# Kernel optimization log

Hardware: AMD Instinct MI355X
Metric: run time of the kernel (lower is better)

## Reference

```python
import jax, jax.numpy as jnp
import numpy as np

N_HEADS = 16
HEAD_DIM = 64
D_MODEL = N_HEADS * HEAD_DIM
NEG_INF = -10000.0


def setup_inputs() -> dict:
    key = jax.random.key(0)
    ks = jax.random.split(key, 6)
    B, S = 2, 2048
    std = 0.02
    return {
        "from_tensor": jax.random.normal(ks[0], (B, S, D_MODEL), dtype=jnp.float32),
        "to_tensor": jax.random.normal(ks[1], (B, S, D_MODEL), dtype=jnp.float32),
        "attention_mask": jnp.ones((B, S, S), dtype=jnp.int32),
        "Wq": jax.random.normal(ks[2], (D_MODEL, D_MODEL), dtype=jnp.float32) * std,
        "bq": jnp.zeros((D_MODEL,), dtype=jnp.float32),
        "Wk": jax.random.normal(ks[3], (D_MODEL, D_MODEL), dtype=jnp.float32) * std,
        "bk": jnp.zeros((D_MODEL,), dtype=jnp.float32),
        "Wv": jax.random.normal(ks[4], (D_MODEL, D_MODEL), dtype=jnp.float32) * std,
        "bv": jnp.zeros((D_MODEL,), dtype=jnp.float32),
    }


def reference(from_tensor, to_tensor, attention_mask, Wq, bq, Wk, bk, Wv, bv):
    B, F, _ = from_tensor.shape
    T = to_tensor.shape[1]
    # Dense QKV projections (no activation by default)
    q = from_tensor @ Wq + bq          # [B, F, N*H]
    k = to_tensor @ Wk + bk            # [B, T, N*H]
    v = to_tensor @ Wv + bv            # [B, T, N*H]
    # split heads -> [B, N, S, H]
    q = q.reshape(B, F, N_HEADS, HEAD_DIM).transpose(0, 2, 1, 3)
    k = k.reshape(B, T, N_HEADS, HEAD_DIM).transpose(0, 2, 1, 3)
    v = v.reshape(B, T, N_HEADS, HEAD_DIM).transpose(0, 2, 1, 3)
    # scaled dot-product scores [B, N, F, T]
    scores = jnp.einsum("bnfh,bnth->bnft", q, k) / jnp.sqrt(jnp.float32(HEAD_DIM))
    # additive mask: (1 - mask) * -10000, broadcast over heads
    adder = (1.0 - attention_mask.astype(jnp.float32))[:, None, :, :] * NEG_INF
    scores = scores + adder
    probs = jax.nn.softmax(scores, axis=-1)  # dropout is identity at inference
    ctx = jnp.einsum("bnft,bnth->bnfh", probs, v)  # [B, N, F, H]
    return ctx.transpose(0, 2, 1, 3).reshape(B, F, N_HEADS * HEAD_DIM)
```

## Files before the change

### kernel.cpp

```cpp
#include <hip/hip_runtime.h>
#include <hip/hip_bf16.h>

typedef unsigned short u16;
typedef __bf16 bf16x8 __attribute__((ext_vector_type(8)));
typedef float f32x4 __attribute__((ext_vector_type(4)));

#define D_MODEL 1024
#define NH 16
#define HD 64
#define SEQ 2048
#define BATCH 2

__device__ __forceinline__ f32x4 mfma16(bf16x8 a, bf16x8 b, f32x4 c) {
    return __builtin_amdgcn_mfma_f32_16x16x32_bf16(a, b, c, 0, 0, 0);
}

__device__ __forceinline__ u16 f2bf(float f) {
    __hip_bfloat16 h = __float2bfloat16(f);
    return *reinterpret_cast<u16*>(&h);
}

__device__ __forceinline__ unsigned cvt_pk_bf16(float lo, float hi) {
    unsigned r;
    asm("v_cvt_pk_bf16_f32 %0, %1, %2" : "=v"(r) : "v"(lo), "v"(hi));
    return r;
}

__device__ __forceinline__ void gload_lds16(const void* g, void* l) {
    __builtin_amdgcn_global_load_lds((__attribute__((address_space(1))) void*)g,
                                     (__attribute__((address_space(3))) void*)l,
                                     16, 0, 0);
}

__global__ __launch_bounds__(256) void prep_k(
    const float* __restrict__ X0, const float* __restrict__ X1,
    u16* __restrict__ Xqc, u16* __restrict__ Xkvc,
    const float* __restrict__ W0, const float* __restrict__ W1,
    const float* __restrict__ W2, u16* __restrict__ Wt,
    const int* __restrict__ mask, int* __restrict__ flags) {
    __shared__ __align__(16) u16 t[64][72];
    const int tid = threadIdx.x;
    int bid = blockIdx.x;

    if (bid < 4096) {
        int i = bid * 256 + tid;
        const float* src = X0; u16* dst = Xqc;
        if (i >= 524288) { src = X1; dst = Xkvc; i -= 524288; }
        const float4 a = ((const float4*)src)[i * 2];
        const float4 b = ((const float4*)src)[i * 2 + 1];
        union { u16 h[8]; uint4 v; } u;
        u.h[0] = f2bf(a.x); u.h[1] = f2bf(a.y); u.h[2] = f2bf(a.z); u.h[3] = f2bf(a.w);
        u.h[4] = f2bf(b.x); u.h[5] = f2bf(b.y); u.h[6] = f2bf(b.z); u.h[7] = f2bf(b.w);
        *(uint4*)(dst + i * 8) = u.v;
        return;
    }
    bid -= 4096;
    if (bid < 768) {
        const int z = bid >> 8, rem = bid & 255;
        const int bx = rem & 15, by = rem >> 4;
        const float* src = (z == 0) ? W0 : (z == 1 ? W1 : W2);
        u16* dst = Wt + (size_t)z * D_MODEL * D_MODEL;
        const int r0 = by * 64, c0 = bx * 64;
#pragma unroll
        for (int j = 0; j < 2; ++j) {
            int idx = j * 256 + tid;
            int rr = idx >> 3, cc = idx & 7;
            size_t base = (size_t)(r0 + rr) * D_MODEL + c0 + cc * 8;
            float4 a = *(const float4*)(src + base);
            float4 b = *(const float4*)(src + base + 4);
            union { u16 h[8]; uint4 v; } u;
            u.h[0] = f2bf(a.x); u.h[1] = f2bf(a.y); u.h[2] = f2bf(a.z); u.h[3] = f2bf(a.w);
            u.h[4] = f2bf(b.x); u.h[5] = f2bf(b.y); u.h[6] = f2bf(b.z); u.h[7] = f2bf(b.w);
            *(uint4*)&t[rr][cc * 8] = u.v;
        }
        __syncthreads();
#pragma unroll
        for (int j = 0; j < 2; ++j) {
            int idx = j * 256 + tid;
            int cc = idx >> 3, rr8 = idx & 7;
            union { u16 h[8]; uint4 v; } u;
#pragma unroll
            for (int e = 0; e < 8; ++e) u.h[e] = t[rr8 * 8 + e][cc];
            *(uint4*)(dst + (size_t)(c0 + cc) * D_MODEL + r0 + rr8 * 8) = u.v;
        }
        return;
    }
    bid -= 768;
    {
        const int ti = bid & 31, fi = (bid >> 5) & 15, b = bid >> 9;
        const int f = fi * 128 + (tid >> 1);
        const int4* p = (const int4*)(mask + ((size_t)(b * SEQ + f)) * SEQ + ti * 64 + (tid & 1) * 32);
        int ok = 1;
#pragma unroll
        for (int j = 0; j < 8; ++j) {
            int4 v = p[j];
            ok &= (v.x == 1) & (v.y == 1) & (v.z == 1) & (v.w == 1);
        }
        __shared__ int sflag;
        if (tid == 0) sflag = 1;
        __syncthreads();
        if (!ok) sflag = 0;
        __syncthreads();
        if (tid == 0) flags[(b * 16 + fi) * 32 + ti] = sflag;
    }
}

__global__ __launch_bounds__(256, 3) void qkv_gemm_k(
    const u16* __restrict__ Xq, const u16* __restrict__ Xkv,
    const u16* __restrict__ Wt,
    const float* __restrict__ bq, const float* __restrict__ bk,
    const float* __restrict__ bv,
    u16* __restrict__ Qb, u16* __restrict__ Kb, u16* __restrict__ Vt) {
    {
    }
    const int lbid = (int)blockIdx.x + 32 * (int)blockIdx.y + 256 * (int)blockIdx.z;
    const int xcd = lbid & 7, j = lbid >> 3;
    const int g = xcd * 3 + (j >> 5);
    const int bx = j & 31, by = g & 7, bz = g >> 3;

    const int z = bz;
    const u16* X = (z == 0) ? Xq : Xkv;
    const u16* Wz = Wt + (size_t)z * D_MODEL * D_MODEL;
    const float* bias = (z == 0) ? bq : (z == 1 ? bk : bv);
    const float scale = (z == 0) ? 0.1803368801111244f : 1.0f;

    __shared__ __align__(16) u16 As[128 * 32];
    __shared__ __align__(16) u16 Bs[128 * 32];

    const int tid = threadIdx.x;
    const int w = tid >> 6, lane = tid & 63;
    const int q = lane >> 4, c = lane & 15;
    const int m0 = bx * 128, n0 = by * 128;
    const int mw = (w & 1) * 64, nw = (w >> 1) * 64;

    f32x4 acc[4][4];
    const f32x4 z4 = {0.f, 0.f, 0.f, 0.f};
#pragma unroll
    for (int mi = 0; mi < 4; ++mi)
#pragma unroll
        for (int ni = 0; ni < 4; ++ni) acc[mi][ni] = z4;

    for (int kb = 0; kb < 32; ++kb) {
        const int k0 = kb * 32;
#pragma unroll
        for (int jj = 0; jj < 2; ++jj) {
            int i = jj * 256 + tid;
            int r = i >> 2, cc = i & 3;
            gload_lds16(X + (size_t)(m0 + r) * D_MODEL + k0 + cc * 8, As + i * 8);
            gload_lds16(Wz + (size_t)(n0 + r) * D_MODEL + k0 + cc * 8, Bs + i * 8);
        }
        __syncthreads();
        bf16x8 af[4], bfr[4];
#pragma unroll
        for (int mi = 0; mi < 4; ++mi)
            af[mi] = *(const bf16x8*)(As + (mw + mi * 16 + c) * 32 + q * 8);
#pragma unroll
        for (int ni = 0; ni < 4; ++ni)
            bfr[ni] = *(const bf16x8*)(Bs + (nw + ni * 16 + c) * 32 + q * 8);
#pragma unroll
        for (int mi = 0; mi < 4; ++mi)
#pragma unroll
            for (int ni = 0; ni < 4; ++ni)
                acc[mi][ni] = mfma16(af[mi], bfr[ni], acc[mi][ni]);
        __syncthreads();
    }

    if (z == 2) {
#pragma unroll
        for (int ni = 0; ni < 4; ++ni) {
            const int colg = n0 + nw + ni * 16 + c;
            const float bvv = bias[colg];
            const int head = colg >> 6, h = colg & 63;
#pragma unroll
            for (int mi = 0; mi < 4; ++mi) {
                const int rowg = m0 + mw + mi * 16 + q * 4;
                const int b = rowg >> 11, s = rowg & 2047;
                union { u16 h4[4]; uint2 v2; } pk;
#pragma unroll
                for (int r = 0; r < 4; ++r) pk.h4[r] = f2bf(acc[mi][ni][r] + bvv);
                *(uint2*)(Vt + (((size_t)(b * NH + head)) * HD + h) * SEQ + s) = pk.v2;
            }
        }
    } else {
        u16* outb = (z == 0) ? Qb : Kb;
#pragma unroll
        for (int ni = 0; ni < 4; ++ni) {
            const int colg = n0 + nw + ni * 16 + c;
            const float bvv = bias[colg];
            const int head = colg >> 6, h = colg & 63;
#pragma unroll
            for (int mi = 0; mi < 4; ++mi) {
                const int rowg = m0 + mw + mi * 16 + q * 4;
#pragma unroll
                for (int r = 0; r < 4; ++r) {
                    const int mrow = rowg + r;
                    const int b = mrow >> 11, s = mrow & 2047;
                    const float val = (acc[mi][ni][r] + bvv) * scale;
                    outb[(((size_t)(b * NH + head)) * SEQ + s) * HD + h] = f2bf(val);
                }
            }
        }
    }
}

#define SWZ(row, off) ((off) ^ (((row) & 7) << 3))
#define SK_OFF (128 * 128)
#define SV_OFF (SK_OFF + 64 * 128)
#define SMEM_BYTES (SV_OFF + 64 * 128)

__global__ __launch_bounds__(256, 4) void attn_k(
    const u16* __restrict__ Qb, const u16* __restrict__ Kb, const u16* __restrict__ Vt,
    const int* __restrict__ flags, const int* __restrict__ mask,
    float* __restrict__ O0, float* __restrict__ l0, float* __restrict__ l1,
    float* __restrict__ out) {
    __shared__ __align__(16) unsigned char smem[SMEM_BYTES];
    const int tid = threadIdx.x;
    const int w = tid >> 6, lane = tid & 63;
    const int q = lane >> 4, c = lane & 15;
    const int lbid = (int)blockIdx.x + 16 * ((int)blockIdx.y + 32 * (int)blockIdx.z);
    const int xcd = lbid & 7, jj = lbid >> 3;
    const int group = xcd * 8 + (jj >> 4);
    const int fi = jj & 15, bn = group & 31, ts = group >> 5;
    const int b = bn >> 4, n = bn & 15;
    const int f0 = fi * 128;

    u16* sQ = (u16*)(smem);
    u16* sK = (u16*)(smem + SK_OFF);
    u16* sV = (u16*)(smem + SV_OFF);
    u16* sP = sQ + w * 32 * 64;

#pragma unroll
    for (int j = 0; j < 4; ++j) {
        int i = j * 256 + tid;
        int r = i >> 3, cc = i & 7;
        uint4 v = *(const uint4*)(Qb + ((size_t)(bn * SEQ + f0 + r)) * HD + cc * 8);
        *(uint4*)(sQ + r * 64 + SWZ(r, cc * 8)) = v;
    }
    __syncthreads();

    bf16x8 qf[2][2];
#pragma unroll
    for (int ft = 0; ft < 2; ++ft)
#pragma unroll
        for (int kb = 0; kb < 2; ++kb)
            qf[ft][kb] = *(const bf16x8*)(sQ + (w * 32 + ft * 16 + c) * 64 + SWZ(c, kb * 32 + q * 8));
    __asm__ __volatile__("" ::: "memory");
    __builtin_amdgcn_s_waitcnt(0xC07F);
    __asm__ __volatile__("" ::: "memory");

    union { u16 h[8]; bf16x8 v; } one_u;
#pragma unroll
    for (int j = 0; j < 8; ++j) one_u.h[j] = 0x3F80;
    const bf16x8 ones = one_u.v;

    f32x4 O[2][4], accL[2];
    const f32x4 z4 = {0.f, 0.f, 0.f, 0.f};
    const f32x4 m10 = {-10.f, -10.f, -10.f, -10.f};
#pragma unroll
    for (int mi = 0; mi < 2; ++mi) {
        accL[mi] = z4;
#pragma unroll
        for (int hi = 0; hi < 4; ++hi) O[mi][hi] = z4;
    }
    const int* flagp = flags + (b * 16 + fi) * 32;

    const int it0 = ts * 16;
    for (int it = it0; it < it0 + 16; ++it) {
        const int t0 = it * 64;
#pragma unroll
        for (int j = 0; j < 2; ++j) {
            int i = j * 256 + tid;
            int r = i >> 3, cc = i & 7;
            uint4 kv = *(const uint4*)(Kb + ((size_t)(bn * SEQ + t0 + r)) * HD + cc * 8);
            uint4 vv = *(const uint4*)(Vt + ((size_t)(bn * HD + r)) * SEQ + t0 + cc * 8);
            const int so = r * 64 + SWZ(r, cc * 8);
            *(uint4*)(sK + so) = kv;
            *(uint4*)(sV + so) = vv;
        }
        __syncthreads();

        const int maskslow = (flagp[it] == 0);

#pragma unroll
        for (int mt = 0; mt < 4; ++mt) {
            bf16x8 kf0 = *(const bf16x8*)(sK + (mt * 16 + c) * 64 + SWZ(c, 0 + q * 8));
            bf16x8 kf1 = *(const bf16x8*)(sK + (mt * 16 + c) * 64 + SWZ(c, 32 + q * 8));
            f32x4 st[2];
            __builtin_amdgcn_s_setprio(1);
#pragma unroll
            for (int ft = 0; ft < 2; ++ft) {
                st[ft] = mfma16(kf0, qf[ft][0], m10);
                st[ft] = mfma16(kf1, qf[ft][1], st[ft]);
            }
            __builtin_amdgcn_s_setprio(0);
            if (maskslow) {
#pragma unroll
                for (int ft = 0; ft < 2; ++ft)
#pragma unroll
                    for (int r = 0; r < 4; ++r) {
                        const int fg = f0 + w * 32 + ft * 16 + c;
                        const int tg = t0 + mt * 16 + q * 4 + r;
                        const int mv = mask[((size_t)(b * SEQ + fg)) * SEQ + tg];
                        st[ft][r] += (1.0f - (float)mv) * (-10000.0f) * 1.4426950408889634f;
                    }
            }
#pragma unroll
            for (int ft = 0; ft < 2; ++ft) {
                uint2 v2;
                v2.x = cvt_pk_bf16(exp2f(st[ft][0]), exp2f(st[ft][1]));
                v2.y = cvt_pk_bf16(exp2f(st[ft][2]), exp2f(st[ft][3]));
                *(uint2*)(sP + (ft * 16 + c) * 64 + SWZ(c, mt * 16 + q * 4)) = v2;
            }
        }
        __asm__ __volatile__("" ::: "memory");
        __builtin_amdgcn_s_waitcnt(0xC07F);
        __asm__ __volatile__("" ::: "memory");

        __builtin_amdgcn_s_setprio(1);
#pragma unroll
        for (int kb = 0; kb < 2; ++kb) {
            bf16x8 pf0 = *(const bf16x8*)(sP + (0 * 16 + c) * 64 + SWZ(c, kb * 32 + q * 8));
            bf16x8 pf1 = *(const bf16x8*)(sP + (1 * 16 + c) * 64 + SWZ(c, kb * 32 + q * 8));
#pragma unroll
            for (int hi = 0; hi < 4; ++hi) {
                bf16x8 vf = *(const bf16x8*)(sV + (hi * 16 + c) * 64 + SWZ(c, kb * 32 + q * 8));
                O[0][hi] = mfma16(pf0, vf, O[0][hi]);
                O[1][hi] = mfma16(pf1, vf, O[1][hi]);
            }
            accL[0] = mfma16(pf0, ones, accL[0]);
            accL[1] = mfma16(pf1, ones, accL[1]);
        }
        __builtin_amdgcn_s_setprio(0);
        __syncthreads();
    }

    float* Odst = ts ? out : O0;
    float* ldst = ts ? l1 : l0;
#pragma unroll
    for (int mi = 0; mi < 2; ++mi)
#pragma unroll
        for (int hi = 0; hi < 4; ++hi)
#pragma unroll
            for (int r = 0; r < 4; ++r) {
                const int fg = f0 + w * 32 + mi * 16 + q * 4 + r;
                const int col = n * 64 + hi * 16 + c;
                Odst[((size_t)(b * SEQ + fg)) * D_MODEL + col] = O[mi][hi][r];
            }
    if (c == 0) {
#pragma unroll
        for (int mi = 0; mi < 2; ++mi)
#pragma unroll
            for (int r = 0; r < 4; ++r) {
                const int fg = f0 + w * 32 + mi * 16 + q * 4 + r;
                ldst[(size_t)bn * SEQ + fg] = accL[mi][r];
            }
    }
}

__global__ __launch_bounds__(256) void combine_k(const float* __restrict__ O0,
                                                 const float* __restrict__ l0,
                                                 const float* __restrict__ l1,
                                                 float* __restrict__ out) {
    const int i = blockIdx.x * 256 + threadIdx.x;
    const int bf = i >> 8;
    const int col = (i & 255) << 2;
    const int n = col >> 6;
    const int lidx = ((bf >> 11) * NH + n) * SEQ + (bf & (SEQ - 1));
    const float inv = 1.0f / (l0[lidx] + l1[lidx]);
    const float4 a = ((const float4*)O0)[i];
    const float4 cpart = ((const float4*)out)[i];
    float4 r;
    r.x = (a.x + cpart.x) * inv;
    r.y = (a.y + cpart.y) * inv;
    r.z = (a.z + cpart.z) * inv;
    r.w = (a.w + cpart.w) * inv;
    ((float4*)out)[i] = r;
}

__global__ __launch_bounds__(256) void signal_k(float* __restrict__ out, int n,
                                                float val) {
    const int i = blockIdx.x * 256 + threadIdx.x;
    if (i < n) out[i] = val;
}

extern "C" void kernel_launch(void* const* d_in, const int* in_sizes, int n_in,
                              void* d_out, int out_size, void* d_ws, size_t ws_size,
                              hipStream_t stream) {
    const float* Xs[2] = {nullptr, nullptr};
    const float* Wp[3] = {nullptr, nullptr, nullptr};
    const float* Bp[3] = {nullptr, nullptr, nullptr};
    const int* mask = nullptr;
    int nx = 0, nw = 0, nb = 0;
    for (int i = 0; i < n_in; ++i) {
        const long long sz = in_sizes[i];
        if (sz == (long long)BATCH * SEQ * D_MODEL) {
            if (nx < 2) Xs[nx++] = (const float*)d_in[i];
        } else if (sz == (long long)BATCH * SEQ * SEQ) {
            mask = (const int*)d_in[i];
        } else if (sz == (long long)D_MODEL * D_MODEL) {
            if (nw < 3) Wp[nw++] = (const float*)d_in[i];
        } else if (sz == (long long)D_MODEL) {
            if (nb < 3) Bp[nb++] = (const float*)d_in[i];
        }
    }
    float* outp = (float*)d_out;
    const size_t MB = 1024 * 1024;
    const size_t NEED = 47 * MB;

    if (ws_size < NEED || nx != 2 || nw != 3 || nb != 3 || !mask) {
        float code = 1000.0f + (float)(ws_size / MB)
                   + (nx != 2 ? 10000.0f : 0.f)
                   + (nw != 3 ? 20000.0f : 0.f)
                   + (nb != 3 ? 40000.0f : 0.f)
                   + (!mask   ? 80000.0f : 0.f);
        signal_k<<<(out_size + 255) / 256, 256, 0, stream>>>(outp, out_size, code);
        return;
    }

    char* ws = (char*)d_ws;
    u16* Xqc   = (u16*)(ws);
    u16* Xkvc  = (u16*)(ws + 8 * MB);
    u16* Wt    = (u16*)(ws + 16 * MB);
    u16* Qb    = (u16*)(ws + 22 * MB);
    u16* Kb    = (u16*)(ws + 30 * MB);
    u16* Vt    = (u16*)(ws + 38 * MB);
    int* flags = (int*)(ws + 46 * MB);
    float* O0 = (float*)(ws);
    float* l0 = (float*)(ws + 46 * MB + 16 * 1024);
    float* l1 = (float*)(ws + 46 * MB + 16 * 1024 + 256 * 1024);

    prep_k<<<5888, 256, 0, stream>>>(Xs[0], Xs[1], Xqc, Xkvc,
                                     Wp[0], Wp[1], Wp[2], Wt, mask, flags);
    qkv_gemm_k<<<dim3(32, 8, 3), 256, 0, stream>>>(Xqc, Xkvc, Wt,
                                                   Bp[0], Bp[1], Bp[2], Qb, Kb, Vt);
    attn_k<<<dim3(16, 32, 2), 256, 0, stream>>>(Qb, Kb, Vt, flags, mask,
                                                O0, l0, l1, outp);
    combine_k<<<4096, 256, 0, stream>>>(O0, l0, l1, outp);
}
```

Baseline: 222.1 us.

## Load K/V fragments directly from global into registers, drop LDS staging and barriers

The attention kernel no longer stages K and V tiles through shared memory. Each lane loads its MFMA operand fragments straight from global memory into registers, which removes the per-iteration __syncthreads barriers and cuts the LDS footprint to the Q/P area. The cost is that each of the four waves now fetches the same K/V data redundantly (relying on L1/L2), and register pressure rises. Because no other wave reads a given wave's P region, only a local waitcnt is kept at the loop end.

```diff
diff --git a/kernel.cpp b/kernel.cpp
--- a/kernel.cpp
+++ b/kernel.cpp
@@ -111,8 +111,6 @@
     const float* __restrict__ bq, const float* __restrict__ bk,
     const float* __restrict__ bv,
     u16* __restrict__ Qb, u16* __restrict__ Kb, u16* __restrict__ Vt) {
-    {
-    }
     const int lbid = (int)blockIdx.x + 32 * (int)blockIdx.y + 256 * (int)blockIdx.z;
     const int xcd = lbid & 7, j = lbid >> 3;
     const int g = xcd * 3 + (j >> 5);
@@ -204,9 +202,7 @@
 }
 
 #define SWZ(row, off) ((off) ^ (((row) & 7) << 3))
-#define SK_OFF (128 * 128)
-#define SV_OFF (SK_OFF + 64 * 128)
-#define SMEM_BYTES (SV_OFF + 64 * 128)
+#define SMEM_BYTES (128 * 128)
 
 __global__ __launch_bounds__(256, 4) void attn_k(
     const u16* __restrict__ Qb, const u16* __restrict__ Kb, const u16* __restrict__ Vt,
@@ -225,8 +221,6 @@
     const int f0 = fi * 128;
 
     u16* sQ = (u16*)(smem);
-    u16* sK = (u16*)(smem + SK_OFF);
-    u16* sV = (u16*)(smem + SV_OFF);
     u16* sP = sQ + w * 32 * 64;
 
 #pragma unroll
@@ -267,24 +261,26 @@
     const int it0 = ts * 16;
     for (int it = it0; it < it0 + 16; ++it) {
         const int t0 = it * 64;
-#pragma unroll
-        for (int j = 0; j < 2; ++j) {
-            int i = j * 256 + tid;
-            int r = i >> 3, cc = i & 7;
-            uint4 kv = *(const uint4*)(Kb + ((size_t)(bn * SEQ + t0 + r)) * HD + cc * 8);
-            uint4 vv = *(const uint4*)(Vt + ((size_t)(bn * HD + r)) * SEQ + t0 + cc * 8);
-            const int so = r * 64 + SWZ(r, cc * 8);
-            *(uint4*)(sK + so) = kv;
-            *(uint4*)(sV + so) = vv;
-        }
-        __syncthreads();
+        uint4 kr0[4], kr1[4], vr0[4], vr1[4];
+#pragma unroll
+        for (int mt = 0; mt < 4; ++mt) {
+            const u16* kp = Kb + ((size_t)(bn * SEQ + t0 + mt * 16 + c)) * HD + q * 8;
+            kr0[mt] = *(const uint4*)(kp);
+            kr1[mt] = *(const uint4*)(kp + 32);
+        }
+#pragma unroll
+        for (int hi = 0; hi < 4; ++hi) {
+            const u16* vp = Vt + ((size_t)(bn * HD + hi * 16 + c)) * SEQ + t0 + q * 8;
+            vr0[hi] = *(const uint4*)(vp);
+            vr1[hi] = *(const uint4*)(vp + 32);
+        }
 
         const int maskslow = (flagp[it] == 0);
 
 #pragma unroll
         for (int mt = 0; mt < 4; ++mt) {
-            bf16x8 kf0 = *(const bf16x8*)(sK + (mt * 16 + c) * 64 + SWZ(c, 0 + q * 8));
-            bf16x8 kf1 = *(const bf16x8*)(sK + (mt * 16 + c) * 64 + SWZ(c, 32 + q * 8));
+            const bf16x8 kf0 = *(const bf16x8*)&kr0[mt];
+            const bf16x8 kf1 = *(const bf16x8*)&kr1[mt];
             f32x4 st[2];
             __builtin_amdgcn_s_setprio(1);
 #pragma unroll
@@ -323,7 +319,8 @@
             bf16x8 pf1 = *(const bf16x8*)(sP + (1 * 16 + c) * 64 + SWZ(c, kb * 32 + q * 8));
 #pragma unroll
             for (int hi = 0; hi < 4; ++hi) {
-                bf16x8 vf = *(const bf16x8*)(sV + (hi * 16 + c) * 64 + SWZ(c, kb * 32 + q * 8));
+                const bf16x8 vf = kb ? *(const bf16x8*)&vr1[hi]
+                                     : *(const bf16x8*)&vr0[hi];
                 O[0][hi] = mfma16(pf0, vf, O[0][hi]);
                 O[1][hi] = mfma16(pf1, vf, O[1][hi]);
             }
@@ -331,7 +328,9 @@
             accL[1] = mfma16(pf1, ones, accL[1]);
         }
         __builtin_amdgcn_s_setprio(0);
-        __syncthreads();
+        __asm__ __volatile__("" ::: "memory");
+        __builtin_amdgcn_s_waitcnt(0xC07F);
+        __asm__ __volatile__("" ::: "memory");
     }
 
     float* Odst = ts ? out : O0;
```

Result: slower. 345.2 us (+55.4%).
